# Kernel tuning notes

Measured on AMD Instinct MI355X. Metric: run time of the kernel, lower is better.

## Reference

```python
import jax, jax.numpy as jnp
import numpy as np

B = 32768
NM = 3      # number of modalities (len(mk))
NE = 8      # number of experts
D_IN = 768
D_P = 128   # per-modality projection dim
D_X = D_P * NM  # 384, concatenated feature dim


def setup_inputs() -> dict:
    key = jax.random.key(0)
    ks = jax.random.split(key, 16)
    s = 0.02
    return {
        "feat_text": jax.random.normal(ks[0], (B, D_IN), jnp.float32),
        "feat_audio": jax.random.normal(ks[1], (B, D_IN), jnp.float32),
        "feat_video": jax.random.normal(ks[2], (B, D_IN), jnp.float32),
        "proj_w": jax.random.normal(ks[3], (NM, D_IN, D_P), jnp.float32) * s,
        "proj_b": jax.random.normal(ks[4], (NM, D_P), jnp.float32) * s,
        "exp_w1": jax.random.normal(ks[5], (NE, D_X, D_P), jnp.float32) * s,
        "exp_b1": jax.random.normal(ks[6], (NE, D_P), jnp.float32) * s,
        "exp_w2": jax.random.normal(ks[7], (NE, D_P, D_P), jnp.float32) * s,
        "exp_b2": jax.random.normal(ks[8], (NE, D_P), jnp.float32) * s,
        "gate_w": jax.random.normal(ks[9], (D_X, NE), jnp.float32) * s,
        "gate_b": jax.random.normal(ks[10], (NE,), jnp.float32) * s,
        "pre_w": jax.random.normal(ks[11], (D_P, 64), jnp.float32) * s,
        "pre_b": jax.random.normal(ks[12], (64,), jnp.float32) * s,
        "head_w": jax.random.normal(ks[13], (64, 2), jnp.float32) * s,
        "head_b": jax.random.normal(ks[14], (2,), jnp.float32) * s,
    }


def reference(feat_text, feat_audio, feat_video, proj_w, proj_b,
              exp_w1, exp_b1, exp_w2, exp_b2, gate_w, gate_b,
              pre_w, pre_b, head_w, head_b):
    feats = jnp.stack([feat_text, feat_audio, feat_video], axis=0)  # [M,B,768]
    # per-modality projections, then concat: [B, 128*M]
    proj = jnp.einsum('mbd,mdp->mbp', feats, proj_w) + proj_b[:, None, :]
    x = jnp.concatenate(jnp.split(proj, NM, axis=0), axis=-1)[0]  # [B, 384]
    # gate: softmax over 8 experts
    gw = jax.nn.softmax(x @ gate_w + gate_b, axis=-1)  # [B, 8]
    # all experts as batched GEMM: [E,B,128]
    h = jax.nn.relu(jnp.einsum('bx,exh->ebh', x, exp_w1) + exp_b1[:, None, :])
    eo = jnp.einsum('ebh,eho->ebo', h, exp_w2) + exp_b2[:, None, :]
    fused = jnp.einsum('be,ebh->bh', gw, eo)  # weighted sum over experts
    penult = jax.nn.relu(fused @ pre_w + pre_b)  # Dropout is identity in eval
    logits = penult @ head_w + head_b  # [B, 2]
    return logits
```

## Files before the change

kernel.cpp:

```cpp
#include <hip/hip_runtime.h>
#include <hip/hip_bf16.h>

#define B_ROWS 32768

typedef unsigned short u16;
typedef unsigned int u32;
typedef float f32x4 __attribute__((ext_vector_type(4)));
typedef __bf16 bf16x8 __attribute__((ext_vector_type(8)));

__device__ __forceinline__ u16 f2bf(float f){
    union { float f; u32 u; } v; v.f = f;
    return (u16)((v.u + 0x7FFFu + ((v.u >> 16) & 1u)) >> 16);
}
__device__ __forceinline__ float bf2f(u16 h){
    union { u32 u; float f; } v; v.u = ((u32)h) << 16; return v.f;
}
__device__ __forceinline__ u32 cvtpk(float lo, float hi){
    u32 r;
    asm("v_cvt_pk_bf16_f32 %0, %1, %2" : "=v"(r) : "v"(lo), "v"(hi));
    return r;
}
__device__ __forceinline__ void async_cp16(void* lds_dst, const void* g_src){
    __builtin_amdgcn_global_load_lds(
        (const __attribute__((address_space(1))) unsigned int*)g_src,
        (__attribute__((address_space(3))) unsigned int*)lds_dst, 16, 0, 0);
}

__global__ void cast_weights_kernel(const float* __restrict__ proj_w,
                                    const float* __restrict__ exp_w1,
                                    const float* __restrict__ exp_w2,
                                    const float* __restrict__ pre_w,
                                    const float* __restrict__ gate_w,
                                    u16* __restrict__ pimg, u16* __restrict__ w1img,
                                    u16* __restrict__ w2img, u16* __restrict__ prwT,
                                    u16* __restrict__ gwimg){
    int i = blockIdx.x * 256 + threadIdx.x;
    if (i < 294912){
        int m = i / 98304, r = i % 98304;
        int c = r / 4096, rr = r % 4096;
        int col = rr >> 5, kk = rr & 31;
        int kb = kk ^ (((col >> 1) & 3) << 3);
        pimg[i] = f2bf(proj_w[m*98304 + (c*32 + kb)*128 + col]);
    } else if (i < 688128){
        int j = i - 294912;
        int e = j / 49152, r = j % 49152;
        int ph = r / 4096, rr = r % 4096;
        int q = rr >> 10, col = (rr >> 3) & 127, el = rr & 7;
        w1img[j] = f2bf(exp_w1[e*49152 + (ph*32 + q*8 + el)*128 + col]);
    } else if (i < 819200){
        int j = i - 688128;
        int e = j / 16384, r = j % 16384;
        int c2 = r / 4096, rr = r % 4096;
        int q = rr >> 10, col = (rr >> 3) & 127, el = rr & 7;
        w2img[j] = f2bf(exp_w2[e*16384 + (c2*32 + q*8 + el)*128 + col]);
    } else if (i < 827392){
        int j = i - 819200;
        int o = j / 128, k = j % 128;
        prwT[j] = f2bf(pre_w[k*64 + o]);
    } else if (i < 833536){
        int j = i - 827392;
        int e = j / 384, k = j % 384;
        gwimg[j] = (e < 8) ? f2bf(gate_w[k*8 + e]) : (u16)0;
    }
}

#define A_OFF    98304
#define B_OFF    147456
#define HS2      0
#define GWT2     32768
#define B1_2     36864
#define B2_2     38912
#define WB2      40960

__global__ __launch_bounds__(512, 1) void fused_kernel(
    const float* __restrict__ ft, const float* __restrict__ fa, const float* __restrict__ fv,
    const u16* __restrict__ pimg, const float* __restrict__ proj_b,
    const u16* __restrict__ w1img, const u16* __restrict__ w2img,
    const u16* __restrict__ prwT, const u16* __restrict__ gwimg,
    const float* __restrict__ gate_b, const float* __restrict__ exp_b1, const float* __restrict__ exp_b2,
    const float* __restrict__ pre_b, const float* __restrict__ head_w, const float* __restrict__ head_b,
    float* __restrict__ out)
{
    __shared__ __align__(16) char lds[163840];
    const int tid = threadIdx.x;
    const int lane = tid & 63, wid = tid >> 6;
    const int wr = wid >> 1, wc = wid & 1;
    const int lr = lane & 15, q = lane >> 4;
    const int blk = blockIdx.x;
    const int row0 = blk * 128;
    const char* w1b = (const char*)w1img;
    const char* w2b = (const char*)w2img;
    char* HsB = lds + HS2;
    u16* b1L = (u16*)(lds + B1_2);
    u16* b2L = (u16*)(lds + B2_2);

    float pb0[4], pb1[4], pb2[4];
    #pragma unroll
    for (int ni = 0; ni < 4; ni++){
        int c = wc*64 + ni*16 + lr;
        pb0[ni] = proj_b[c];
        pb1[ni] = proj_b[128 + c];
        pb2[ni] = proj_b[256 + c];
    }
    asm volatile("s_waitcnt vmcnt(0)" ::: "memory");

    u32 aoffs[2];
    #pragma unroll
    for (int i = 0; i < 2; i++){
        int P = i*8192 + tid*16;
        int row = P >> 7, inner = P & 127;
        aoffs[i] = (u32)((row0 + row)*3072 + (inner ^ ((row & 7) << 4)));
    }

#define ASTAGE(c) do{                                                          \
        int mm_ = (c) / 24, kk_ = (c) % 24;                                    \
        const char* ab_ = (const char*)(mm_ == 0 ? ft : mm_ == 1 ? fa : fv);   \
        char* la_ = lds + A_OFF + ((c) % 3)*16384 + tid*16;                    \
        async_cp16(la_,        ab_ + aoffs[0] + kk_*128);                      \
        async_cp16(la_ + 8192, ab_ + aoffs[1] + kk_*128);                      \
    }while(0)

#define BSTAGE(c) do{                                                          \
        int mm_ = (c) / 24, kk_ = (c) % 24;                                    \
        async_cp16(lds + B_OFF + ((c) % 2)*8192 + tid*16,                      \
                   (const char*)pimg + mm_*196608 + kk_*8192 + tid*16);        \
    }while(0)

#define PCONSUME(c) do{                                                        \
        const char* Abuf = lds + A_OFF + ((c) % 3)*16384;                      \
        const char* Bbuf = lds + B_OFF + ((c) % 2)*8192;                       \
        bf16x8 af[2];                                                          \
        _Pragma("unroll")                                                      \
        for (int mi = 0; mi < 2; mi++){                                        \
            int row = wr*32 + mi*16 + lr;                                      \
            int aoff = row*128 + ((q*32) ^ ((row & 7) << 4));                  \
            f32x4 a0 = *(const f32x4*)(Abuf + aoff);                           \
            f32x4 a1 = *(const f32x4*)(Abuf + (aoff ^ 16));                    \
            union { u32 w[4]; bf16x8 v; } u;                                   \
            u.w[0] = cvtpk(a0.x, a0.y); u.w[1] = cvtpk(a0.z, a0.w);            \
            u.w[2] = cvtpk(a1.x, a1.y); u.w[3] = cvtpk(a1.z, a1.w);            \
            af[mi] = u.v;                                                      \
        }                                                                      \
        __builtin_amdgcn_s_setprio(1);                                         \
        _Pragma("unroll")                                                      \
        for (int ni = 0; ni < 4; ni++){                                        \
            int col = wc*64 + ni*16 + lr;                                      \
            int boff = col*64 + ((q*16) ^ (((col >> 1) & 3) << 4));            \
            bf16x8 bf = *(const bf16x8*)(Bbuf + boff);                         \
            acc[0][ni] = __builtin_amdgcn_mfma_f32_16x16x32_bf16(af[0], bf, acc[0][ni], 0, 0, 0); \
            acc[1][ni] = __builtin_amdgcn_mfma_f32_16x16x32_bf16(af[1], bf, acc[1][ni], 0, 0, 0); \
        }                                                                      \
        __builtin_amdgcn_s_setprio(0);                                         \
    }while(0)

#define PHASE_A_MOD(MC, PB) do{                                                \
        _Pragma("unroll 1")                                                    \
        for (int kt = 0; kt < 24; kt++){                                       \
            int t = MC*24 + kt;                                                \
            __builtin_amdgcn_sched_barrier(0);                                 \
            __builtin_amdgcn_s_barrier();                                      \
            if (t < 71) BSTAGE(t + 1);                                         \
            if (t < 70) ASTAGE(t + 2);                                         \
            if (t < 70)       asm volatile("s_waitcnt vmcnt(5)" ::: "memory"); \
            else if (t == 70) asm volatile("s_waitcnt vmcnt(3)" ::: "memory"); \
            else              asm volatile("s_waitcnt vmcnt(0)" ::: "memory"); \
            __builtin_amdgcn_s_barrier();                                      \
            __builtin_amdgcn_sched_barrier(0);                                 \
            PCONSUME(t);                                                       \
        }                                                                      \
        _Pragma("unroll")                                                      \
        for (int mi = 0; mi < 2; mi++)                                         \
            _Pragma("unroll")                                                  \
            for (int ni = 0; ni < 4; ni++){                                    \
                int lcol = wc*64 + ni*16 + lr;                                 \
                int colg = MC*128 + lcol;                                      \
                int ktI = colg >> 5, qI = (colg >> 3) & 3, el = colg & 7;      \
                _Pragma("unroll")                                              \
                for (int j = 0; j < 4; j++){                                   \
                    int row = wr*32 + mi*16 + q*4 + j;                         \
                    *(u16*)(lds + (row >> 6)*49152 + ktI*4096 + qI*1024        \
                            + (row & 63)*16 + el*2) = f2bf(acc[mi][ni][j] + PB[ni]); \
                    acc[mi][ni][j] = 0.f;                                      \
                }                                                              \
            }                                                                  \
    }while(0)

    f32x4 acc[2][4];
    #pragma unroll
    for (int i = 0; i < 2; i++)
        #pragma unroll
        for (int j = 0; j < 4; j++) acc[i][j] = {0.f, 0.f, 0.f, 0.f};

    BSTAGE(0); ASTAGE(0); ASTAGE(1);
    PHASE_A_MOD(0, pb0);
    PHASE_A_MOD(1, pb1);
    PHASE_A_MOD(2, pb2);
#undef ASTAGE
#undef BSTAGE
#undef PCONSUME
#undef PHASE_A_MOD

    asm volatile("s_waitcnt lgkmcnt(0)" ::: "memory");
    __builtin_amdgcn_sched_barrier(0);
    __builtin_amdgcn_s_barrier();

    bf16x8 xreg[12][2];
    {
        const char* xa0 = lds + (wr >> 1)*49152 + q*1024;
        #pragma unroll
        for (int ph = 0; ph < 12; ph++){
            xreg[ph][0] = *(const bf16x8*)(xa0 + ph*4096 + ((wr & 1)*32 + lr)*16);
            xreg[ph][1] = *(const bf16x8*)(xa0 + ph*4096 + ((wr & 1)*32 + 16 + lr)*16);
        }
    }
    float gw4[4];
    {
        f32x4 ga = {0.f, 0.f, 0.f, 0.f};
        const char* xb = lds + (wid >> 2)*49152 + ((wid & 3)*16 + lr)*16 + q*1024;
        const u16* gwp = gwimg + lr*384 + q*8;
        #pragma unroll
        for (int kt = 0; kt < 12; kt++){
            bf16x8 af = *(const bf16x8*)(xb + kt*4096);
            bf16x8 gb = *(const bf16x8*)(gwp + kt*32);
            ga = __builtin_amdgcn_mfma_f32_16x16x32_bf16(af, gb, ga, 0, 0, 0);
        }
        float gbv = gate_b[lr & 7];
        #pragma unroll
        for (int j = 0; j < 4; j++){
            float v = ga[j] + gbv;
            float mx = v;
            mx = fmaxf(mx, __shfl_xor(mx, 1));
            mx = fmaxf(mx, __shfl_xor(mx, 2));
            mx = fmaxf(mx, __shfl_xor(mx, 4));
            float s = __expf(v - mx);
            float t = s;
            t += __shfl_xor(t, 1);
            t += __shfl_xor(t, 2);
            t += __shfl_xor(t, 4);
            gw4[j] = s / t;
        }
    }
    asm volatile("s_waitcnt lgkmcnt(0)" ::: "memory");
    __builtin_amdgcn_sched_barrier(0);
    __builtin_amdgcn_s_barrier();

#define WGROUP_STAGE2(gg2, sl) do{                                             \
        int e2_ = (gg2) / 6, i2_ = (gg2) % 6;                                  \
        char* dst_ = lds + WB2 + (sl)*24576 + tid*16;                          \
        if (i2_ < 4){                                                          \
            const char* src_ = w1b + e2_*98304 + i2_*24576 + tid*16;           \
            async_cp16(dst_,         src_);                                    \
            async_cp16(dst_ + 8192,  src_ + 8192);                             \
            async_cp16(dst_ + 16384, src_ + 16384);                            \
        } else {                                                               \
            const char* src_ = w2b + e2_*32768 + (i2_ - 4)*16384 + tid*16;     \
            async_cp16(dst_,         src_);                                    \
            async_cp16(dst_ + 8192,  src_ + 8192);                             \
            async_cp16(dst_ + 16384, src_);            \
        }                                                                      \
    }while(0)

    if (lr < 8){
        f32x4 wv = {gw4[0], gw4[1], gw4[2], gw4[3]};
        *(f32x4*)(lds + GWT2 + lr*512 + (wid*16 + q*4)*4) = wv;
    }
    for (int i = tid; i < 1024; i += 512){
        b1L[i] = f2bf(exp_b1[i]);
        b2L[i] = f2bf(exp_b2[i]);
    }
    WGROUP_STAGE2(0, 0);
    WGROUP_STAGE2(1, 1);
    asm volatile("s_waitcnt vmcnt(0) lgkmcnt(0)" ::: "memory");
    __builtin_amdgcn_sched_barrier(0);
    __builtin_amdgcn_s_barrier();

    f32x4 fus[2][4];
    #pragma unroll
    for (int i = 0; i < 2; i++)
        #pragma unroll
        for (int j = 0; j < 4; j++) fus[i][j] = {0.f, 0.f, 0.f, 0.f};

    #pragma unroll 1
    for (int e = 0; e < 8; e++){
        f32x4 ac1[2][4];
        #pragma unroll
        for (int i = 0; i < 2; i++)
            #pragma unroll
            for (int j = 0; j < 4; j++) ac1[i][j] = {0.f, 0.f, 0.f, 0.f};

        #pragma unroll
        for (int grp = 0; grp < 4; grp++){
            int g = e*6 + grp;
            const char* wbase = lds + WB2 + (g & 1)*24576;
            __builtin_amdgcn_s_setprio(1);
            #pragma unroll
            for (int c = 0; c < 3; c++){
                int ph = grp*3 + c;
                const char* wsl = wbase + c*8192 + q*2048;
                #pragma unroll
                for (int ni = 0; ni < 4; ni++){
                    bf16x8 bf = *(const bf16x8*)(wsl + (wc*64 + ni*16 + lr)*16);
                    ac1[0][ni] = __builtin_amdgcn_mfma_f32_16x16x32_bf16(xreg[ph][0], bf, ac1[0][ni], 0, 0, 0);
                    ac1[1][ni] = __builtin_amdgcn_mfma_f32_16x16x32_bf16(xreg[ph][1], bf, ac1[1][ni], 0, 0, 0);
                }
            }
            __builtin_amdgcn_s_setprio(0);
            if (grp == 3){
                #pragma unroll
                for (int mi = 0; mi < 2; mi++)
                    #pragma unroll
                    for (int ni = 0; ni < 4; ni++){
                        int col = wc*64 + ni*16 + lr;
                        float b1v = bf2f(b1L[e*128 + col]);
                        #pragma unroll
                        for (int j = 0; j < 4; j++){
                            int row = wr*32 + mi*16 + q*4 + j;
                            *(u16*)(HsB + row*256 + ((col*2) ^ ((row & 7) << 4)))
                                = f2bf(fmaxf(ac1[mi][ni][j] + b1v, 0.f));
                        }
                    }
                asm volatile("s_waitcnt lgkmcnt(0)" ::: "memory");
            }
            __builtin_amdgcn_sched_barrier(0);
            __builtin_amdgcn_s_barrier();
            {
                int gn = g + 2;
                if (gn < 48){
                    WGROUP_STAGE2(gn, gn & 1);
                    asm volatile("s_waitcnt vmcnt(3)" ::: "memory");
                } else {
                    asm volatile("s_waitcnt vmcnt(0)" ::: "memory");
                }
            }
            __builtin_amdgcn_s_barrier();
            __builtin_amdgcn_sched_barrier(0);
        }

        f32x4 ac2[2][4];
        #pragma unroll
        for (int i = 0; i < 2; i++)
            #pragma unroll
            for (int j = 0; j < 4; j++) ac2[i][j] = {0.f, 0.f, 0.f, 0.f};

        #pragma unroll 1
        for (int grp = 0; grp < 2; grp++){
            int g = e*6 + 4 + grp;
            const char* wbase = lds + WB2 + (g & 1)*24576;
            #pragma unroll
            for (int c = 0; c < 2; c++){
                int p2 = grp*2 + c;
                const char* wsl = wbase + c*8192 + q*2048;
                int cb = p2*64 + q*16;
                int rowA = wr*32 + lr;
                int rowB = wr*32 + 16 + lr;
                bf16x8 af0 = *(const bf16x8*)(HsB + rowA*256 + (cb ^ ((rowA & 7) << 4)));
                bf16x8 af1 = *(const bf16x8*)(HsB + rowB*256 + (cb ^ ((rowB & 7) << 4)));
                __builtin_amdgcn_s_setprio(1);
                #pragma unroll
                for (int ni = 0; ni < 4; ni++){
                    bf16x8 bf = *(const bf16x8*)(wsl + (wc*64 + ni*16 + lr)*16);
                    ac2[0][ni] = __builtin_amdgcn_mfma_f32_16x16x32_bf16(af0, bf, ac2[0][ni], 0, 0, 0);
                    ac2[1][ni] = __builtin_amdgcn_mfma_f32_16x16x32_bf16(af1, bf, ac2[1][ni], 0, 0, 0);
                }
                __builtin_amdgcn_s_setprio(0);
            }
            __builtin_amdgcn_sched_barrier(0);
            __builtin_amdgcn_s_barrier();
            {
                int gn = g + 2;
                if (gn < 48){
                    WGROUP_STAGE2(gn, gn & 1);
                    asm volatile("s_waitcnt vmcnt(3)" ::: "memory");
                } else {
                    asm volatile("s_waitcnt vmcnt(0)" ::: "memory");
                }
            }
            __builtin_amdgcn_s_barrier();
            __builtin_amdgcn_sched_barrier(0);
        }
        #pragma unroll
        for (int mi = 0; mi < 2; mi++){
            f32x4 gwv = *(const f32x4*)(lds + GWT2 + e*512 + (wr*32 + mi*16 + q*4)*4);
            #pragma unroll
            for (int ni = 0; ni < 4; ni++){
                int col = wc*64 + ni*16 + lr;
                float b2v = bf2f(b2L[e*128 + col]);
                #pragma unroll
                for (int j = 0; j < 4; j++)
                    fus[mi][ni][j] += gwv[j] * (ac2[mi][ni][j] + b2v);
            }
        }
    }
#undef WGROUP_STAGE2

    __builtin_amdgcn_sched_barrier(0);
    __builtin_amdgcn_s_barrier();
    #pragma unroll
    for (int mi = 0; mi < 2; mi++)
        #pragma unroll
        for (int ni = 0; ni < 4; ni++){
            int col = wc*64 + ni*16 + lr;
            #pragma unroll
            for (int j = 0; j < 4; j++){
                int row = wr*32 + mi*16 + q*4 + j;
                *(u16*)(HsB + row*256 + ((col*2) ^ ((row & 7) << 4))) = f2bf(fus[mi][ni][j]);
            }
        }
    asm volatile("s_waitcnt lgkmcnt(0)" ::: "memory");
    __builtin_amdgcn_sched_barrier(0);
    __builtin_amdgcn_s_barrier();

    f32x4 ap[4];
    #pragma unroll
    for (int i = 0; i < 4; i++) ap[i] = {0.f, 0.f, 0.f, 0.f};
    #pragma unroll
    for (int kt = 0; kt < 4; kt++){
        int row = wid*16 + lr;
        int cb = kt*64 + q*16;
        bf16x8 af = *(const bf16x8*)(HsB + row*256 + (cb ^ ((row & 7) << 4)));
        #pragma unroll
        for (int ni = 0; ni < 4; ni++){
            bf16x8 bf = *(const bf16x8*)(prwT + (size_t)(ni*16 + lr)*128 + kt*32 + q*8);
            ap[ni] = __builtin_amdgcn_mfma_f32_16x16x32_bf16(af, bf, ap[ni], 0, 0, 0);
        }
    }
    float* Pen = (float*)(lds + WB2);
    #pragma unroll
    for (int ni = 0; ni < 4; ni++){
        int col = ni*16 + lr;
        float pbv = pre_b[col];
        #pragma unroll
        for (int j = 0; j < 4; j++){
            int row = wid*16 + q*4 + j;
            Pen[row*68 + col] = fmaxf(ap[ni][j] + pbv, 0.f);
        }
    }
    asm volatile("s_waitcnt lgkmcnt(0)" ::: "memory");
    __builtin_amdgcn_sched_barrier(0);
    __builtin_amdgcn_s_barrier();
    if (tid < 256){
        int r = tid >> 1, c = tid & 1;
        float s = head_b[c];
        #pragma unroll 8
        for (int k = 0; k < 64; k++) s += Pen[r*68 + k] * head_w[k*2 + c];
        out[(size_t)(blk*128 + r)*2 + c] = s;
    }
}

extern "C" void kernel_launch(void* const* d_in, const int* in_sizes, int n_in,
                              void* d_out, int out_size, void* d_ws, size_t ws_size,
                              hipStream_t stream) {
    const float* ft     = (const float*)d_in[0];
    const float* fa     = (const float*)d_in[1];
    const float* fv     = (const float*)d_in[2];
    const float* proj_w = (const float*)d_in[3];
    const float* proj_b = (const float*)d_in[4];
    const float* exp_w1 = (const float*)d_in[5];
    const float* exp_b1 = (const float*)d_in[6];
    const float* exp_w2 = (const float*)d_in[7];
    const float* exp_b2 = (const float*)d_in[8];
    const float* gate_w = (const float*)d_in[9];
    const float* gate_b = (const float*)d_in[10];
    const float* pre_w  = (const float*)d_in[11];
    const float* pre_b  = (const float*)d_in[12];
    const float* head_w = (const float*)d_in[13];
    const float* head_b = (const float*)d_in[14];
    float* out = (float*)d_out;

    u16* pimg  = (u16*)d_ws;
    u16* w1img = pimg + 294912;
    u16* w2img = w1img + 393216;
    u16* prwT  = w2img + 131072;
    u16* gwimg = prwT + 8192;

    cast_weights_kernel<<<3256, 256, 0, stream>>>(proj_w, exp_w1, exp_w2, pre_w, gate_w,
                                                  pimg, w1img, w2img, prwT, gwimg);
    fused_kernel<<<256, 512, 0, stream>>>(ft, fa, fv, pimg, proj_b,
                                          w1img, w2img, prwT, gwimg,
                                          gate_b, exp_b1, exp_b2,
                                          pre_b, head_w, head_b, out);
}
```

Measured before the change: 104.2 us.

## Double-stage projection pipeline in pairs and load x fragments per modality

The projection GEMM pipeline now stages two k-steps of A and B per group and syncs once per pair, which halves the barrier count. The x tile is written to a small per-modality LDS slice and read into registers after each modality, freeing LDS and removing the final bulk reload. The gate GEMM reuses the x registers and computes both 16-row halves per wave, so redundant LDS reads and a barrier go away. In exchange, prefetch depth and the LDS buffer layout change, and each modality end adds extra barriers.

```diff
diff --git a/kernel.cpp b/kernel.cpp
--- a/kernel.cpp
+++ b/kernel.cpp
@@ -64,8 +64,9 @@
     }
 }
 
-#define A_OFF    98304
-#define B_OFF    147456
+#define XSL      0
+#define A2       32768
+#define B2       98304
 #define HS2      0
 #define GWT2     32768
 #define B1_2     36864
@@ -112,23 +113,27 @@
         aoffs[i] = (u32)((row0 + row)*3072 + (inner ^ ((row & 7) << 4)));
     }
 
-#define ASTAGE(c) do{                                                          \
-        int mm_ = (c) / 24, kk_ = (c) % 24;                                    \
+    bf16x8 xreg[12][2];
+
+#define STAGE_GROUP(G) do{                                                     \
+        int mm_ = (G)/12, kk0_ = ((G)%12)*2;                                   \
         const char* ab_ = (const char*)(mm_ == 0 ? ft : mm_ == 1 ? fa : fv);   \
-        char* la_ = lds + A_OFF + ((c) % 3)*16384 + tid*16;                    \
-        async_cp16(la_,        ab_ + aoffs[0] + kk_*128);                      \
-        async_cp16(la_ + 8192, ab_ + aoffs[1] + kk_*128);                      \
+        int sb_ = ((G)&1)*2;                                                   \
+        char* a0_ = lds + A2 + sb_*16384 + tid*16;                             \
+        char* a1_ = a0_ + 16384;                                               \
+        const char* bs_ = (const char*)pimg + mm_*196608 + kk0_*8192 + tid*16; \
+        async_cp16(a0_,        ab_ + aoffs[0] + kk0_*128);                     \
+        async_cp16(a0_ + 8192, ab_ + aoffs[1] + kk0_*128);                     \
+        async_cp16(lds + B2 + sb_*8192 + tid*16, bs_);                         \
+        async_cp16(a1_,        ab_ + aoffs[0] + (kk0_+1)*128);                 \
+        async_cp16(a1_ + 8192, ab_ + aoffs[1] + (kk0_+1)*128);                 \
+        async_cp16(lds + B2 + (sb_+1)*8192 + tid*16, bs_ + 8192);              \
     }while(0)
 
-#define BSTAGE(c) do{                                                          \
-        int mm_ = (c) / 24, kk_ = (c) % 24;                                    \
-        async_cp16(lds + B_OFF + ((c) % 2)*8192 + tid*16,                      \
-                   (const char*)pimg + mm_*196608 + kk_*8192 + tid*16);        \
-    }while(0)
-
-#define PCONSUME(c) do{                                                        \
-        const char* Abuf = lds + A_OFF + ((c) % 3)*16384;                      \
-        const char* Bbuf = lds + B_OFF + ((c) % 2)*8192;                       \
+#define CONSUME1(c) do{                                                        \
+        int sl_ = (((c) >> 1) & 1)*2 + ((c) & 1);                              \
+        const char* Abuf = lds + A2 + sl_*16384;                               \
+        const char* Bbuf = lds + B2 + sl_*8192;                                \
         bf16x8 af[2];                                                          \
         _Pragma("unroll")                                                      \
         for (int mi = 0; mi < 2; mi++){                                        \
@@ -155,34 +160,49 @@
 
 #define PHASE_A_MOD(MC, PB) do{                                                \
         _Pragma("unroll 1")                                                    \
-        for (int kt = 0; kt < 24; kt++){                                       \
-            int t = MC*24 + kt;                                                \
+        for (int grp = 0; grp < 12; grp++){                                    \
+            int G = MC*12 + grp;                                               \
             __builtin_amdgcn_sched_barrier(0);                                 \
-            __builtin_amdgcn_s_barrier();                                      \
-            if (t < 71) BSTAGE(t + 1);                                         \
-            if (t < 70) ASTAGE(t + 2);                                         \
-            if (t < 70)       asm volatile("s_waitcnt vmcnt(5)" ::: "memory"); \
-            else if (t == 70) asm volatile("s_waitcnt vmcnt(3)" ::: "memory"); \
-            else              asm volatile("s_waitcnt vmcnt(0)" ::: "memory"); \
-            __builtin_amdgcn_s_barrier();                                      \
+            CONSUME1(2*G);                                                     \
+            CONSUME1(2*G + 1);                                                 \
             __builtin_amdgcn_sched_barrier(0);                                 \
-            PCONSUME(t);                                                       \
+            __builtin_amdgcn_s_barrier();       \
+            if (MC < 2 || grp < 10){                                           \
+                STAGE_GROUP(G + 2);             \
+                asm volatile("s_waitcnt vmcnt(6)" ::: "memory");   \
+            } else {                                                           \
+                asm volatile("s_waitcnt vmcnt(0)" ::: "memory");               \
+            }                                                                  \
+            __builtin_amdgcn_s_barrier();              \
+            __builtin_amdgcn_sched_barrier(0);                                 \
         }                                                                      \
+                                  \
         _Pragma("unroll")                                                      \
         for (int mi = 0; mi < 2; mi++)                                         \
             _Pragma("unroll")                                                  \
             for (int ni = 0; ni < 4; ni++){                                    \
                 int lcol = wc*64 + ni*16 + lr;                                 \
-                int colg = MC*128 + lcol;                                      \
-                int ktI = colg >> 5, qI = (colg >> 3) & 3, el = colg & 7;      \
+                int ktL = lcol >> 5, qI = (lcol >> 3) & 3, el = lcol & 7;      \
                 _Pragma("unroll")                                              \
                 for (int j = 0; j < 4; j++){                                   \
                     int row = wr*32 + mi*16 + q*4 + j;                         \
-                    *(u16*)(lds + (row >> 6)*49152 + ktI*4096 + qI*1024        \
+                    *(u16*)(lds + XSL + (row >> 6)*16384 + ktL*4096 + qI*1024  \
                             + (row & 63)*16 + el*2) = f2bf(acc[mi][ni][j] + PB[ni]); \
                     acc[mi][ni][j] = 0.f;                                      \
                 }                                                              \
             }                                                                  \
+        asm volatile("s_waitcnt lgkmcnt(0)" ::: "memory");                     \
+        __builtin_amdgcn_sched_barrier(0);                                     \
+        __builtin_amdgcn_s_barrier();                                          \
+        {                      \
+            const char* xa0 = lds + XSL + (wr >> 1)*16384 + q*1024;            \
+            _Pragma("unroll")                                                  \
+            for (int ph = 0; ph < 4; ph++){                                    \
+                xreg[MC*4 + ph][0] = *(const bf16x8*)(xa0 + ph*4096 + ((wr & 1)*32 + lr)*16);      \
+                xreg[MC*4 + ph][1] = *(const bf16x8*)(xa0 + ph*4096 + ((wr & 1)*32 + 16 + lr)*16); \
+            }                                                                  \
+        }                                                                      \
+        asm volatile("s_waitcnt lgkmcnt(0)" ::: "memory");                     \
     }while(0)
 
     f32x4 acc[2][4];
@@ -191,58 +211,51 @@
         #pragma unroll
         for (int j = 0; j < 4; j++) acc[i][j] = {0.f, 0.f, 0.f, 0.f};
 
-    BSTAGE(0); ASTAGE(0); ASTAGE(1);
+    STAGE_GROUP(0);
+    STAGE_GROUP(1);
+    asm volatile("s_waitcnt vmcnt(6)" ::: "memory");
+    __builtin_amdgcn_sched_barrier(0);
+    __builtin_amdgcn_s_barrier();
     PHASE_A_MOD(0, pb0);
     PHASE_A_MOD(1, pb1);
     PHASE_A_MOD(2, pb2);
-#undef ASTAGE
-#undef BSTAGE
-#undef PCONSUME
+#undef STAGE_GROUP
+#undef CONSUME1
 #undef PHASE_A_MOD
 
-    asm volatile("s_waitcnt lgkmcnt(0)" ::: "memory");
-    __builtin_amdgcn_sched_barrier(0);
-    __builtin_amdgcn_s_barrier();
-
-    bf16x8 xreg[12][2];
+    float gw4a[4], gw4b[4];
     {
-        const char* xa0 = lds + (wr >> 1)*49152 + q*1024;
+        f32x4 ga0 = {0.f,0.f,0.f,0.f}, ga1 = {0.f,0.f,0.f,0.f};
+        const u16* gwp = gwimg + lr*384 + q*8;
         #pragma unroll
         for (int ph = 0; ph < 12; ph++){
-            xreg[ph][0] = *(const bf16x8*)(xa0 + ph*4096 + ((wr & 1)*32 + lr)*16);
-            xreg[ph][1] = *(const bf16x8*)(xa0 + ph*4096 + ((wr & 1)*32 + 16 + lr)*16);
-        }
-    }
-    float gw4[4];
-    {
-        f32x4 ga = {0.f, 0.f, 0.f, 0.f};
-        const char* xb = lds + (wid >> 2)*49152 + ((wid & 3)*16 + lr)*16 + q*1024;
-        const u16* gwp = gwimg + lr*384 + q*8;
-        #pragma unroll
-        for (int kt = 0; kt < 12; kt++){
-            bf16x8 af = *(const bf16x8*)(xb + kt*4096);
-            bf16x8 gb = *(const bf16x8*)(gwp + kt*32);
-            ga = __builtin_amdgcn_mfma_f32_16x16x32_bf16(af, gb, ga, 0, 0, 0);
+            bf16x8 gb = *(const bf16x8*)(gwp + ph*32);
+            ga0 = __builtin_amdgcn_mfma_f32_16x16x32_bf16(xreg[ph][0], gb, ga0, 0, 0, 0);
+            ga1 = __builtin_amdgcn_mfma_f32_16x16x32_bf16(xreg[ph][1], gb, ga1, 0, 0, 0);
         }
         float gbv = gate_b[lr & 7];
         #pragma unroll
         for (int j = 0; j < 4; j++){
-            float v = ga[j] + gbv;
+            float v = ga0[j] + gbv;
             float mx = v;
             mx = fmaxf(mx, __shfl_xor(mx, 1));
             mx = fmaxf(mx, __shfl_xor(mx, 2));
             mx = fmaxf(mx, __shfl_xor(mx, 4));
             float s = __expf(v - mx);
             float t = s;
-            t += __shfl_xor(t, 1);
-            t += __shfl_xor(t, 2);
-            t += __shfl_xor(t, 4);
-            gw4[j] = s / t;
-        }
-    }
-    asm volatile("s_waitcnt lgkmcnt(0)" ::: "memory");
-    __builtin_amdgcn_sched_barrier(0);
-    __builtin_amdgcn_s_barrier();
+            t += __shfl_xor(t, 1); t += __shfl_xor(t, 2); t += __shfl_xor(t, 4);
+            gw4a[j] = s / t;
+            float v1 = ga1[j] + gbv;
+            float mx1 = v1;
+            mx1 = fmaxf(mx1, __shfl_xor(mx1, 1));
+            mx1 = fmaxf(mx1, __shfl_xor(mx1, 2));
+            mx1 = fmaxf(mx1, __shfl_xor(mx1, 4));
+            float s1 = __expf(v1 - mx1);
+            float t1 = s1;
+            t1 += __shfl_xor(t1, 1); t1 += __shfl_xor(t1, 2); t1 += __shfl_xor(t1, 4);
+            gw4b[j] = s1 / t1;
+        }
+    }
 
 #define WGROUP_STAGE2(gg2, sl) do{                                             \
         int e2_ = (gg2) / 6, i2_ = (gg2) % 6;                                  \
@@ -260,9 +273,11 @@
         }                                                                      \
     }while(0)
 
-    if (lr < 8){
-        f32x4 wv = {gw4[0], gw4[1], gw4[2], gw4[3]};
-        *(f32x4*)(lds + GWT2 + lr*512 + (wid*16 + q*4)*4) = wv;
+    if (wc == 0 && lr < 8){
+        f32x4 wa = {gw4a[0], gw4a[1], gw4a[2], gw4a[3]};
+        f32x4 wb = {gw4b[0], gw4b[1], gw4b[2], gw4b[3]};
+        *(f32x4*)(lds + GWT2 + lr*512 + (wr*32 + q*4)*4) = wa;
+        *(f32x4*)(lds + GWT2 + lr*512 + (wr*32 + 16 + q*4)*4) = wb;
     }
     for (int i = tid; i < 1024; i += 512){
         b1L[i] = f2bf(exp_b1[i]);
```

Result: slower. 106.5 us (+2.3%).
